# Kernel optimization log

Measured on AMD Instinct MI355X. Metric: run time of the kernel, lower is better.

The kernel has to match this reference:

```python
import jax, jax.numpy as jnp
import numpy as np

DIM = 192
HEADS = 8
TIME = 256
HID = int(DIM * 2.66)  # 510
B, H, W = 4, 128, 128


def conv1x1(x, w, b):
    # w: [O, C], pointwise conv as einsum
    return jnp.einsum('bchw,oc->bohw', x, w) + b[None, :, None, None]


def dwconv3(x, w, b):
    # depthwise 3x3, w: [C, 1, 3, 3]
    y = jax.lax.conv_general_dilated(
        x, w, window_strides=(1, 1), padding='SAME',
        feature_group_count=x.shape[1],
        dimension_numbers=('NCHW', 'OIHW', 'NCHW'))
    return y + b[None, :, None, None]


def layernorm(x, w, b, eps=1e-6):
    # channel-wise LN; torch .std() is unbiased (ddof=1)
    C = x.shape[1]
    mean = x.mean(axis=1, keepdims=True)
    var = ((x - mean) ** 2).sum(axis=1, keepdims=True) / (C - 1)
    std = jnp.sqrt(var)
    return w * (x - mean) / (std + eps) + b


def modulate(x, t_emb, tw, tb):
    # time_mlp = Linear(SiLU(t_emb)); scale/shift conditioning
    t = jax.nn.silu(t_emb) @ tw.T + tb  # [B, 2C]
    scale, shift = jnp.split(t, 2, axis=-1)
    return x * (1.0 + scale[:, :, None, None]) + shift[:, :, None, None]


def l2norm(x, eps=1e-12):
    n = jnp.sqrt((x * x).sum(axis=-1, keepdims=True))
    return x / jnp.maximum(n, eps)


def mdta(x, t_emb, temp, qkv_w, qkv_b, dw_w, dw_b, proj_w, proj_b, tw, tb):
    Bn, C, Hh, Ww = x.shape
    x = modulate(x, t_emb, tw, tb)
    qkv = dwconv3(conv1x1(x, qkv_w, qkv_b), dw_w, dw_b)
    q, k, v = jnp.split(qkv, 3, axis=1)
    rs = lambda a: a.reshape(Bn, HEADS, C // HEADS, Hh * Ww)
    q, k, v = l2norm(rs(q)), l2norm(rs(k)), rs(v)
    attn = jnp.einsum('bhcl,bhdl->bhcd', q, k) * temp[None]  # [B,h,c,c]
    attn = jax.nn.softmax(attn, axis=-1)
    out = jnp.einsum('bhcd,bhdl->bhcl', attn, v).reshape(Bn, C, Hh, Ww)
    return conv1x1(out, proj_w, proj_b)


def gdfn(x, t_emb, c1_w, c1_b, dw_w, dw_b, c2_w, c2_b, tw, tb):
    x = modulate(x, t_emb, tw, tb)
    x = dwconv3(conv1x1(x, c1_w, c1_b), dw_w, dw_b)
    x1, x2 = jnp.split(x, 2, axis=1)
    return conv1x1(x1 * x2, c2_w, c2_b)


def setup_inputs() -> dict:
    key = jax.random.key(0)
    ks = jax.random.split(key, 16)
    s = 0.02
    d = {
        'x': jax.random.normal(ks[0], (B, DIM, H, W), jnp.float32),
        't_emb': jax.random.normal(ks[1], (B, TIME), jnp.float32),
        'n1_w': jnp.ones((1, DIM, 1, 1), jnp.float32),
        'n1_b': jnp.zeros((1, DIM, 1, 1), jnp.float32),
        'temp': jnp.ones((HEADS, 1, 1), jnp.float32),
        'a_qkv_w': jax.random.normal(ks[2], (3 * DIM, DIM), jnp.float32) * s,
        'a_qkv_b': jnp.zeros((3 * DIM,), jnp.float32),
        'a_dw_w': jax.random.normal(ks[3], (3 * DIM, 1, 3, 3), jnp.float32) * s,
        'a_dw_b': jnp.zeros((3 * DIM,), jnp.float32),
        'a_proj_w': jax.random.normal(ks[4], (DIM, DIM), jnp.float32) * s,
        'a_proj_b': jnp.zeros((DIM,), jnp.float32),
        'a_t_w': jax.random.normal(ks[5], (2 * DIM, TIME), jnp.float32) * s,
        'a_t_b': jnp.zeros((2 * DIM,), jnp.float32),
        'n2_w': jnp.ones((1, DIM, 1, 1), jnp.float32),
        'n2_b': jnp.zeros((1, DIM, 1, 1), jnp.float32),
        'f_c1_w': jax.random.normal(ks[6], (2 * HID, DIM), jnp.float32) * s,
        'f_c1_b': jnp.zeros((2 * HID,), jnp.float32),
        'f_dw_w': jax.random.normal(ks[7], (2 * HID, 1, 3, 3), jnp.float32) * s,
        'f_dw_b': jnp.zeros((2 * HID,), jnp.float32),
        'f_c2_w': jax.random.normal(ks[8], (DIM, HID), jnp.float32) * s,
        'f_c2_b': jnp.zeros((DIM,), jnp.float32),
        'f_t_w': jax.random.normal(ks[9], (2 * DIM, TIME), jnp.float32) * s,
        'f_t_b': jnp.zeros((2 * DIM,), jnp.float32),
    }
    return d


def reference(x, t_emb, n1_w, n1_b, temp, a_qkv_w, a_qkv_b, a_dw_w, a_dw_b,
              a_proj_w, a_proj_b, a_t_w, a_t_b, n2_w, n2_b,
              f_c1_w, f_c1_b, f_dw_w, f_dw_b, f_c2_w, f_c2_b, f_t_w, f_t_b):
    x = x + mdta(layernorm(x, n1_w, n1_b), t_emb, temp,
                 a_qkv_w, a_qkv_b, a_dw_w, a_dw_b, a_proj_w, a_proj_b, a_t_w, a_t_b)
    x = x + gdfn(layernorm(x, n2_w, n2_b), t_emb,
                 f_c1_w, f_c1_b, f_dw_w, f_dw_b, f_c2_w, f_c2_b, f_t_w, f_t_b)
    return x
```

## Files before the change

### kernel.cpp

```cpp
#include <hip/hip_runtime.h>
#include <math.h>

#define HW 16384

using short8 = __attribute__((ext_vector_type(8))) short;
using f32x4  = __attribute__((ext_vector_type(4))) float;

__device__ __forceinline__ float bf2f(unsigned short u){
  union { unsigned int i; float f; } x; x.i = ((unsigned int)u) << 16; return x.f;
}
__device__ __forceinline__ unsigned short f2bf(float f){
  union { float f; unsigned int i; } x; x.f = f;
  return (unsigned short)((x.i + 0x7FFFu + ((x.i >> 16) & 1u)) >> 16);
}

__global__ void castw_k(const float* __restrict__ in, unsigned short* __restrict__ out, int n){
  int i = blockIdx.x * 256 + threadIdx.x;
  if (i < n) out[i] = f2bf(in[i]);
}
__global__ void castw_pad_k(const float* __restrict__ in, unsigned short* __restrict__ out,
                            int M, int Kin, int Kout){
  int i = blockIdx.x * 256 + threadIdx.x;
  if (i < M * Kout){
    int m = i / Kout, k = i - m * Kout;
    out[i] = (k < Kin) ? f2bf(in[m * Kin + k]) : (unsigned short)0;
  }
}

__global__ void modk(const float* __restrict__ t_emb,
                     const float* __restrict__ aw, const float* __restrict__ ab,
                     const float* __restrict__ fw, const float* __restrict__ fb,
                     float* __restrict__ mod_a, float* __restrict__ mod_f){
  int o = blockIdx.x * 128 + threadIdx.x;
  int b = blockIdx.y;
  const float* w  = blockIdx.z ? fw : aw;
  const float* bi = blockIdx.z ? fb : ab;
  float* outp     = blockIdx.z ? mod_f : mod_a;
  const float* te = t_emb + b * 256;
  float acc = bi[o];
  for (int k = 0; k < 256; ++k){
    float u = te[k];
    float s = u / (1.f + expf(-u));
    acc += s * w[o * 256 + k];
  }
  outp[b * 384 + o] = acc;
}

__global__ __launch_bounds__(256) void lnmod_k(const float* __restrict__ x,
                                               const float* __restrict__ nw, const float* __restrict__ nb,
                                               const float* __restrict__ mod, unsigned short* __restrict__ y){
  int b = blockIdx.y;
  int p = blockIdx.x * 256 + threadIdx.x;
  const float* xb = x + (size_t)b * 192 * HW + p;
  float s = 0.f, s2 = 0.f;
  #pragma unroll 8
  for (int c = 0; c < 192; ++c){
    float v = xb[(size_t)c * HW]; s += v; s2 += v * v;
  }
  float mean = s * (1.f / 192.f);
  float var  = (s2 - s * mean) * (1.f / 191.f);
  float rinv = 1.f / (sqrtf(fmaxf(var, 0.f)) + 1e-6f);
  const float* mo = mod + b * 384;
  unsigned short* yb = y + ((size_t)b * HW + p) * 192;
  #pragma unroll
  for (int c8 = 0; c8 < 24; ++c8){
    unsigned short ob[8];
    #pragma unroll
    for (int j = 0; j < 8; ++j){
      int c = c8 * 8 + j;
      float v = xb[(size_t)c * HW];
      float ln = nw[c] * ((v - mean) * rinv) + nb[c];
      ob[j] = f2bf(ln * (1.f + mo[c]) + mo[192 + c]);
    }
    *(uint4*)(yb + c8 * 8) = *(const uint4*)ob;
  }
}

__global__ __launch_bounds__(256, 2) void gemm_tn2(const unsigned short* __restrict__ A,
                                                   const unsigned short* __restrict__ Bact,
                                                   const float* __restrict__ bias,
                                                   const float* resid, void* outp,
                                                   int M, int K, int ofp32){
  const int N = HW;
  __shared__ unsigned short SMEM[20480];
  const int m0 = blockIdx.x * 64;
  const int n0 = blockIdx.y * 256;
  const int bz = blockIdx.z;
  const unsigned short* Bp = Bact + (size_t)bz * N * K;
  const int t = threadIdx.x;
  const int w = t >> 6, lane = t & 63;
  const int l16 = lane & 15, quad = lane >> 4;

  const int arow = t >> 2, akc = t & 3;
  int gm = m0 + arow; if (gm > M - 1) gm = M - 1;
  const unsigned short* agp = A + (size_t)gm * K + akc * 8;
  const int aoff = arow * 32 + ((akc ^ ((arow ^ (arow >> 2)) & 3)) * 8);
  const int brow = t >> 2, bkc = t & 3;
  const unsigned short* bgp = Bp + (size_t)(n0 + brow) * K + bkc * 8;
  const int bslot = (bkc ^ ((brow ^ (brow >> 2)) & 3)) * 8;

  f32x4 acc[4][4];
  #pragma unroll
  for (int i = 0; i < 4; ++i)
    #pragma unroll
    for (int j = 0; j < 4; ++j) acc[i][j] = (f32x4){0.f, 0.f, 0.f, 0.f};

  const int kTiles = K >> 5;
  {
    uint4 va = *(const uint4*)agp;
    *(uint4*)&SMEM[aoff] = va;
    #pragma unroll
    for (int i = 0; i < 4; ++i){
      uint4 vb = *(const uint4*)(bgp + (size_t)(64 * i) * K);
      *(uint4*)&SMEM[4096 + (brow + 64 * i) * 32 + bslot] = vb;
    }
  }
  __syncthreads();

  const int fs = (quad ^ ((l16 ^ (l16 >> 2)) & 3)) * 8;
  for (int kt = 0; kt < kTiles; ++kt){
    const int cur = kt & 1;
    const bool more = (kt + 1 < kTiles);
    uint4 va; uint4 vb[4];
    if (more){
      const int k0 = (kt + 1) * 32;
      va = *(const uint4*)(agp + k0);
      #pragma unroll
      for (int i = 0; i < 4; ++i)
        vb[i] = *(const uint4*)(bgp + (size_t)(64 * i) * K + k0);
    }
    const int abase = cur * 2048;
    const int bbase = 4096 + cur * 8192;
    short8 af[4], bfr[4];
    #pragma unroll
    for (int mt = 0; mt < 4; ++mt)
      af[mt] = *(const short8*)&SMEM[abase + (mt * 16 + l16) * 32 + fs];
    #pragma unroll
    for (int nt = 0; nt < 4; ++nt)
      bfr[nt] = *(const short8*)&SMEM[bbase + (w * 64 + nt * 16 + l16) * 32 + fs];
    #pragma unroll
    for (int nt = 0; nt < 4; ++nt)
      #pragma unroll
      for (int mt = 0; mt < 4; ++mt)
        acc[mt][nt] = __builtin_amdgcn_mfma_f32_16x16x32_bf16(af[mt], bfr[nt], acc[mt][nt], 0, 0, 0);
    if (more){
      const int nabase = (cur ^ 1) * 2048;
      const int nbbase = 4096 + (cur ^ 1) * 8192;
      *(uint4*)&SMEM[nabase + aoff] = va;
      #pragma unroll
      for (int i = 0; i < 4; ++i)
        *(uint4*)&SMEM[nbbase + (brow + 64 * i) * 32 + bslot] = vb[i];
    }
    __syncthreads();
  }

  if (!ofp32){
    unsigned short* T = SMEM;
    #pragma unroll
    for (int mt = 0; mt < 4; ++mt)
      #pragma unroll
      for (int nt = 0; nt < 4; ++nt)
        #pragma unroll
        for (int r = 0; r < 4; ++r){
          int ml = mt * 16 + quad * 4 + r;
          int bm = m0 + ml; if (bm > M - 1) bm = M - 1;
          T[ml * 264 + w * 64 + nt * 16 + l16] = f2bf(acc[mt][nt][r] + bias[bm]);
        }
    __syncthreads();
    unsigned short* ob = (unsigned short*)outp + (size_t)bz * M * N;
    #pragma unroll
    for (int i = 0; i < 8; ++i){
      int c = t + 256 * i;
      int row = c >> 5, col = (c & 31) * 8;
      if (m0 + row < M)
        *(uint4*)(ob + (size_t)(m0 + row) * N + n0 + col) = *(const uint4*)&T[row * 264 + col];
    }
  } else {
    float* T = (float*)&SMEM[0];
    float* ob = (float*)outp + (size_t)bz * M * N;
    const float* rb = resid ? resid + (size_t)bz * M * N : nullptr;
    #pragma unroll
    for (int half = 0; half < 2; ++half){
      #pragma unroll
      for (int mt = 0; mt < 2; ++mt)
        #pragma unroll
        for (int nt = 0; nt < 4; ++nt)
          #pragma unroll
          for (int r = 0; r < 4; ++r){
            int ml = mt * 16 + quad * 4 + r;
            T[ml * 260 + w * 64 + nt * 16 + l16] = acc[half * 2 + mt][nt][r];
          }
      __syncthreads();
      #pragma unroll
      for (int i = 0; i < 8; ++i){
        int c = t + 256 * i;
        int row = c >> 6, col = (c & 63) * 4;
        int m = m0 + half * 32 + row;
        if (m < M){
          size_t idx = (size_t)m * N + n0 + col;
          f32x4 v = *(const f32x4*)&T[row * 260 + col];
          float bv = bias[m];
          v[0] += bv; v[1] += bv; v[2] += bv; v[3] += bv;
          if (rb){
            v[0] += rb[idx]; v[1] += rb[idx + 1]; v[2] += rb[idx + 2]; v[3] += rb[idx + 3];
          }
          *(f32x4*)&ob[idx] = v;
        }
      }
      __syncthreads();
    }
  }
}

__global__ __launch_bounds__(256) void dw3_k(const unsigned short* __restrict__ in,
                                             const float* __restrict__ w, const float* __restrict__ bias,
                                             unsigned short* __restrict__ out, int C,
                                             float* __restrict__ qn, float* __restrict__ kn){
  __shared__ unsigned short tile[66 * 128];
  __shared__ float red[4];
  int zc = blockIdx.y;
  int b = zc / C, c = zc - b * C;
  int r0 = blockIdx.x * 64;
  const unsigned short* im = in + ((size_t)(b * C + c)) * HW;
  unsigned short* om = out + ((size_t)(b * C + c)) * HW;
  int t = threadIdx.x;
  #pragma unroll
  for (int i = 0; i < 5; ++i){
    int idx = t + 256 * i;
    if (idx < 1056){
      int lr = idx >> 4, lc = (idx & 15) * 8;
      int gr = r0 - 1 + lr;
      uint4 v = {0u, 0u, 0u, 0u};
      if ((unsigned)gr < 128u) v = *(const uint4*)(im + gr * 128 + lc);
      *(uint4*)&tile[lr * 128 + lc] = v;
    }
  }
  __syncthreads();
  const float* wc = w + c * 9;
  float W[9];
  #pragma unroll
  for (int i = 0; i < 9; ++i) W[i] = wc[i];
  float bs = bias[c];
  float ssq = 0.f;
  #pragma unroll
  for (int i = 0; i < 4; ++i){
    int seg = t + 256 * i;
    int orow = seg >> 4, sc = (seg & 15) * 8;
    float acc[8];
    #pragma unroll
    for (int j = 0; j < 8; ++j) acc[j] = bs;
    #pragma unroll
    for (int rr = 0; rr < 3; ++rr){
      const unsigned short* rp = &tile[(orow + rr) * 128 + sc];
      float v[10];
      v[0] = (sc > 0) ? bf2f(rp[-1]) : 0.f;
      uint4 m = *(const uint4*)rp;
      const unsigned short* mu = (const unsigned short*)&m;
      #pragma unroll
      for (int j = 0; j < 8; ++j) v[j + 1] = bf2f(mu[j]);
      v[9] = (sc < 120) ? bf2f(rp[8]) : 0.f;
      float wa = W[rr * 3], wb = W[rr * 3 + 1], wd = W[rr * 3 + 2];
      #pragma unroll
      for (int j = 0; j < 8; ++j) acc[j] += wa * v[j] + wb * v[j + 1] + wd * v[j + 2];
    }
    unsigned short ob[8];
    #pragma unroll
    for (int j = 0; j < 8; ++j){
      ob[j] = f2bf(acc[j]);
      float q = bf2f(ob[j]);
      ssq += q * q;
    }
    *(uint4*)(om + (r0 + orow) * 128 + sc) = *(uint4*)ob;
  }
  if (c < 384){
    #pragma unroll
    for (int off = 32; off; off >>= 1) ssq += __shfl_down(ssq, off);
    if ((t & 63) == 0) red[t >> 6] = ssq;
    __syncthreads();
    if (t == 0){
      float s = red[0] + red[1] + red[2] + red[3];
      float* dst = (c < 192) ? (qn + b * 192 + c) : (kn + b * 192 + c - 192);
      atomicAdd(dst, s);
    }
  }
}

__global__ __launch_bounds__(256) void dwgate_k(const unsigned short* __restrict__ h,
                                                const float* __restrict__ w, const float* __restrict__ bias,
                                                unsigned short* __restrict__ g){
  __shared__ unsigned short tile[2 * 66 * 128];
  int zc = blockIdx.y;
  int b = zc / 510, j = zc - b * 510;
  int r0 = blockIdx.x * 64;
  const unsigned short* im1 = h + ((size_t)(b * 1020 + j)) * HW;
  const unsigned short* im2 = h + ((size_t)(b * 1020 + 510 + j)) * HW;
  int t = threadIdx.x;
  #pragma unroll
  for (int i = 0; i < 9; ++i){
    int idx = t + 256 * i;
    if (idx < 2112){
      int img = (idx >= 1056) ? 1 : 0;
      int li = idx - img * 1056;
      int lr = li >> 4, lc = (li & 15) * 8;
      int gr = r0 - 1 + lr;
      uint4 v = {0u, 0u, 0u, 0u};
      const unsigned short* im = img ? im2 : im1;
      if ((unsigned)gr < 128u) v = *(const uint4*)(im + gr * 128 + lc);
      *(uint4*)&tile[img * 8448 + lr * 128 + lc] = v;
    }
  }
  __syncthreads();
  float W1[9], W2[9];
  #pragma unroll
  for (int i = 0; i < 9; ++i){ W1[i] = w[j * 9 + i]; W2[i] = w[(510 + j) * 9 + i]; }
  float b1 = bias[j], b2 = bias[510 + j];
  unsigned short* gm = g + ((size_t)(b * 510 + j)) * HW;
  #pragma unroll
  for (int i = 0; i < 4; ++i){
    int seg = t + 256 * i;
    int orow = seg >> 4, sc = (seg & 15) * 8;
    float a1[8], a2[8];
    #pragma unroll
    for (int q = 0; q < 8; ++q){ a1[q] = b1; a2[q] = b2; }
    #pragma unroll
    for (int rr = 0; rr < 3; ++rr){
      #pragma unroll
      for (int img = 0; img < 2; ++img){
        const unsigned short* rp = &tile[img * 8448 + (orow + rr) * 128 + sc];
        float v[10];
        v[0] = (sc > 0) ? bf2f(rp[-1]) : 0.f;
        uint4 m = *(const uint4*)rp;
        const unsigned short* mu = (const unsigned short*)&m;
        #pragma unroll
        for (int q = 0; q < 8; ++q) v[q + 1] = bf2f(mu[q]);
        v[9] = (sc < 120) ? bf2f(rp[8]) : 0.f;
        const float* ww = img ? W2 : W1;
        float* aa = img ? a2 : a1;
        float wa = ww[rr * 3], wb = ww[rr * 3 + 1], wd = ww[rr * 3 + 2];
        #pragma unroll
        for (int q = 0; q < 8; ++q) aa[q] += wa * v[q] + wb * v[q + 1] + wd * v[q + 2];
      }
    }
    unsigned short ob[8];
    #pragma unroll
    for (int q = 0; q < 8; ++q) ob[q] = f2bf(a1[q] * a2[q]);
    *(uint4*)(gm + (r0 + orow) * 128 + sc) = *(uint4*)ob;
  }
}

__global__ __launch_bounds__(256) void tr_k(const unsigned short* __restrict__ in,
                                            unsigned short* __restrict__ out, int C, int Kout){
  __shared__ unsigned short tile[64 * 72];
  int b = blockIdx.z;
  int p0 = blockIdx.x * 64, c0 = blockIdx.y * 64;
  int t = threadIdx.x;
  #pragma unroll
  for (int i = 0; i < 2; ++i){
    int id = t + 256 * i;
    int ch = id >> 3, pc = (id & 7) * 8;
    uint4 v = {0u, 0u, 0u, 0u};
    if (c0 + ch < C) v = *(const uint4*)(in + ((size_t)(b * C + c0 + ch)) * HW + p0 + pc);
    const unsigned short* u = (const unsigned short*)&v;
    #pragma unroll
    for (int j = 0; j < 8; ++j) tile[(pc + j) * 72 + ch] = u[j];
  }
  __syncthreads();
  #pragma unroll
  for (int i = 0; i < 2; ++i){
    int id = t + 256 * i;
    int px = id >> 3, cc = (id & 7) * 8;
    *(uint4*)(out + ((size_t)b * HW + p0 + px) * Kout + c0 + cc) = *(const uint4*)&tile[px * 72 + cc];
  }
}

__global__ __launch_bounds__(64) void qk_k(const unsigned short* __restrict__ qkv_dw, float* __restrict__ part){
  int bh = blockIdx.y; int b = bh >> 3, h = bh & 7;
  int ks = blockIdx.x;
  int lane = threadIdx.x;
  int l16 = lane & 15, quad = lane >> 4;
  const unsigned short* qb = qkv_dw + ((size_t)b * 576 + h * 24) * HW;
  const unsigned short* kb = qkv_dw + ((size_t)b * 576 + 192 + h * 24) * HW;
  f32x4 z = {0.f, 0.f, 0.f, 0.f};
  f32x4 a00 = z, a01 = z, a10 = z, a11 = z;
  for (int st = 0; st < 16; ++st){
    int k0 = ks * 512 + st * 32 + quad * 8;
    short8 qa0 = *(const short8*)(qb + (size_t)l16 * HW + k0);
    short8 qa1 = *(const short8*)(qb + (size_t)(l16 + 16) * HW + k0);
    short8 kb0 = *(const short8*)(kb + (size_t)l16 * HW + k0);
    short8 kb1 = *(const short8*)(kb + (size_t)(l16 + 16) * HW + k0);
    a00 = __builtin_amdgcn_mfma_f32_16x16x32_bf16(qa0, kb0, a00, 0, 0, 0);
    a01 = __builtin_amdgcn_mfma_f32_16x16x32_bf16(qa0, kb1, a01, 0, 0, 0);
    a10 = __builtin_amdgcn_mfma_f32_16x16x32_bf16(qa1, kb0, a10, 0, 0, 0);
    a11 = __builtin_amdgcn_mfma_f32_16x16x32_bf16(qa1, kb1, a11, 0, 0, 0);
  }
  float* pp = part + ((size_t)bh * 32 + ks) * 576;
  #pragma unroll
  for (int r = 0; r < 4; ++r){
    int c0 = quad * 4 + r, c1 = 16 + quad * 4 + r;
    int d0 = l16, d1 = 16 + l16;
    if (c0 < 24 && d0 < 24) pp[c0 * 24 + d0] = a00[r];
    if (c0 < 24 && d1 < 24) pp[c0 * 24 + d1] = a01[r];
    if (c1 < 24 && d0 < 24) pp[c1 * 24 + d0] = a10[r];
    if (c1 < 24 && d1 < 24) pp[c1 * 24 + d1] = a11[r];
  }
}

__global__ void softmax_k(const float* __restrict__ part, const float* __restrict__ qn,
                          const float* __restrict__ kn, const float* __restrict__ temp,
                          float* __restrict__ attn){
  int bh = blockIdx.x; int b = bh >> 3, h = bh & 7;
  int c = threadIdx.x;
  if (c >= 24) return;
  float tmp = temp[h];
  float qv = fmaxf(sqrtf(qn[b * 192 + h * 24 + c]), 1e-12f);
  float row[24];
  #pragma unroll
  for (int d = 0; d < 24; ++d){
    float s = 0.f;
    for (int sp = 0; sp < 32; ++sp) s += part[((size_t)bh * 32 + sp) * 576 + c * 24 + d];
    float kv = fmaxf(sqrtf(kn[b * 192 + h * 24 + d]), 1e-12f);
    row[d] = s * tmp / (qv * kv);
  }
  float mx = row[0];
  #pragma unroll
  for (int d = 1; d < 24; ++d) mx = fmaxf(mx, row[d]);
  float sum = 0.f;
  #pragma unroll
  for (int d = 0; d < 24; ++d){ row[d] = expf(row[d] - mx); sum += row[d]; }
  float inv = 1.f / sum;
  #pragma unroll
  for (int d = 0; d < 24; ++d) attn[(size_t)bh * 576 + c * 24 + d] = row[d] * inv;
}

__global__ __launch_bounds__(256) void av_k(const float* __restrict__ attn,
                                            const unsigned short* __restrict__ qkv_dw,
                                            unsigned short* __restrict__ o){
  int bh = blockIdx.y; int b = bh >> 3, h = bh & 7;
  __shared__ float As[576];
  int t = threadIdx.x;
  for (int i = t; i < 576; i += 256) As[i] = attn[(size_t)bh * 576 + i];
  __syncthreads();
  int p = blockIdx.x * 256 + t;
  const unsigned short* vb = qkv_dw + ((size_t)b * 576 + 384 + h * 24) * HW + p;
  float acc[24];
  #pragma unroll
  for (int c = 0; c < 24; ++c) acc[c] = 0.f;
  #pragma unroll
  for (int d = 0; d < 24; ++d){
    float vv = bf2f(vb[(size_t)d * HW]);
    #pragma unroll
    for (int c = 0; c < 24; ++c) acc[c] += As[c * 24 + d] * vv;
  }
  unsigned short ob[24];
  #pragma unroll
  for (int c = 0; c < 24; ++c) ob[c] = f2bf(acc[c]);
  unsigned short* op = o + ((size_t)b * HW + p) * 192 + h * 24;
  #pragma unroll
  for (int i = 0; i < 3; ++i) *(uint4*)(op + i * 8) = *(const uint4*)(ob + i * 8);
}

extern "C" void kernel_launch(void* const* d_in, const int* in_sizes, int n_in,
                              void* d_out, int out_size, void* d_ws, size_t ws_size,
                              hipStream_t stream){
  (void)in_sizes; (void)n_in; (void)out_size; (void)ws_size;
  const float* x        = (const float*)d_in[0];
  const float* t_emb    = (const float*)d_in[1];
  const float* n1_w     = (const float*)d_in[2];
  const float* n1_b     = (const float*)d_in[3];
  const float* temp     = (const float*)d_in[4];
  const float* a_qkv_w  = (const float*)d_in[5];
  const float* a_qkv_b  = (const float*)d_in[6];
  const float* a_dw_w   = (const float*)d_in[7];
  const float* a_dw_b   = (const float*)d_in[8];
  const float* a_proj_w = (const float*)d_in[9];
  const float* a_proj_b = (const float*)d_in[10];
  const float* a_t_w    = (const float*)d_in[11];
  const float* a_t_b    = (const float*)d_in[12];
  const float* n2_w     = (const float*)d_in[13];
  const float* n2_b     = (const float*)d_in[14];
  const float* f_c1_w   = (const float*)d_in[15];
  const float* f_c1_b   = (const float*)d_in[16];
  const float* f_dw_w   = (const float*)d_in[17];
  const float* f_dw_b   = (const float*)d_in[18];
  const float* f_c2_w   = (const float*)d_in[19];
  const float* f_c2_b   = (const float*)d_in[20];
  const float* f_t_w    = (const float*)d_in[21];
  const float* f_t_b    = (const float*)d_in[22];
  float* out = (float*)d_out;
  char* ws = (char*)d_ws;

  unsigned short* y_buf = (unsigned short*)(ws + 0);
  unsigned short* qkv   = (unsigned short*)(ws + 25165824);
  unsigned short* hbuf  = (unsigned short*)(ws + 25165824);
  unsigned short* gbufT = (unsigned short*)(ws + 25165824);
  unsigned short* qkvd  = (unsigned short*)(ws + 100663296);
  unsigned short* obuf  = (unsigned short*)(ws + 176160768);
  unsigned short* gbuf  = (unsigned short*)(ws + 158859264);
  const size_t S = 225705984;
  float* mod_a = (float*)(ws + S);
  float* mod_f = (float*)(ws + S + 8192);
  float* qn    = (float*)(ws + S + 16384);
  float* kn    = (float*)(ws + S + 20480);
  float* part  = (float*)(ws + S + 24576);
  float* attn  = (float*)(ws + S + 2383872);
  unsigned short* Wq  = (unsigned short*)(ws + S + 2457600);
  unsigned short* Wp  = (unsigned short*)(ws + S + 2678784);
  unsigned short* W1  = (unsigned short*)(ws + S + 2752512);
  unsigned short* W2p = (unsigned short*)(ws + S + 3144192);

  castw_k<<<dim3((110592 + 255) / 256), 256, 0, stream>>>(a_qkv_w, Wq, 110592);
  castw_k<<<dim3((36864 + 255) / 256), 256, 0, stream>>>(a_proj_w, Wp, 36864);
  castw_k<<<dim3((195840 + 255) / 256), 256, 0, stream>>>(f_c1_w, W1, 195840);
  castw_pad_k<<<dim3((98304 + 255) / 256), 256, 0, stream>>>(f_c2_w, W2p, 192, 510, 512);
  modk<<<dim3(3, 4, 2), 128, 0, stream>>>(t_emb, a_t_w, a_t_b, f_t_w, f_t_b, mod_a, mod_f);
  (void)hipMemsetAsync(qn, 0, 2 * 768 * sizeof(float), stream);

  lnmod_k<<<dim3(64, 4), 256, 0, stream>>>(x, n1_w, n1_b, mod_a, y_buf);
  gemm_tn2<<<dim3(9, 64, 4), 256, 0, stream>>>(Wq, y_buf, a_qkv_b, nullptr, qkv, 576, 192, 0);
  dw3_k<<<dim3(2, 2304), 256, 0, stream>>>(qkv, a_dw_w, a_dw_b, qkvd, 576, qn, kn);
  qk_k<<<dim3(32, 32), 64, 0, stream>>>(qkvd, part);
  softmax_k<<<32, 64, 0, stream>>>(part, qn, kn, temp, attn);
  av_k<<<dim3(64, 32), 256, 0, stream>>>(attn, qkvd, obuf);
  gemm_tn2<<<dim3(3, 64, 4), 256, 0, stream>>>(Wp, obuf, a_proj_b, x, out, 192, 192, 1);

  lnmod_k<<<dim3(64, 4), 256, 0, stream>>>(out, n2_w, n2_b, mod_f, y_buf);
  gemm_tn2<<<dim3(16, 64, 4), 256, 0, stream>>>(W1, y_buf, f_c1_b, nullptr, hbuf, 1020, 192, 0);
  dwgate_k<<<dim3(2, 2040), 256, 0, stream>>>(hbuf, f_dw_w, f_dw_b, gbuf);
  tr_k<<<dim3(256, 8, 4), 256, 0, stream>>>(gbuf, gbufT, 510, 512);
  gemm_tn2<<<dim3(3, 64, 4), 256, 0, stream>>>(W2p, gbufT, f_c2_b, out, out, 192, 512, 1);
}
```

Baseline: 780.4 us.

## Retile pointwise GEMM to 256 output channels by 64 pixels per block

Changes the bf16 MFMA GEMM block tile from 64 output channels by 256 pixels to 256 channels by 64 pixels. Each wave now owns 64 channel rows instead of 64 pixel columns, and the shared-memory staging and both epilogues are reworked to match. Launch grids shrink along the channel axis and grow along the pixel axis. The large activation matrix is therefore re-read fewer times, at the cost of wasted MFMA work on padded channel rows when M is 192 or 576, and shorter 128-byte row segments in the output stores.

```diff
diff --git a/kernel.cpp b/kernel.cpp
--- a/kernel.cpp
+++ b/kernel.cpp
@@ -83,8 +83,8 @@
                                                    int M, int K, int ofp32){
   const int N = HW;
   __shared__ unsigned short SMEM[20480];
-  const int m0 = blockIdx.x * 64;
-  const int n0 = blockIdx.y * 256;
+  const int m0 = blockIdx.x * 256;
+  const int n0 = blockIdx.y * 64;
   const int bz = blockIdx.z;
   const unsigned short* Bp = Bact + (size_t)bz * N * K;
   const int t = threadIdx.x;
@@ -92,12 +92,16 @@
   const int l16 = lane & 15, quad = lane >> 4;
 
   const int arow = t >> 2, akc = t & 3;
-  int gm = m0 + arow; if (gm > M - 1) gm = M - 1;
-  const unsigned short* agp = A + (size_t)gm * K + akc * 8;
+  const unsigned short* agp[4];
+  #pragma unroll
+  for (int i = 0; i < 4; ++i){
+    int gm = m0 + arow + 64 * i; if (gm > M - 1) gm = M - 1;
+    agp[i] = A + (size_t)gm * K + akc * 8;
+  }
   const int aoff = arow * 32 + ((akc ^ ((arow ^ (arow >> 2)) & 3)) * 8);
   const int brow = t >> 2, bkc = t & 3;
   const unsigned short* bgp = Bp + (size_t)(n0 + brow) * K + bkc * 8;
-  const int bslot = (bkc ^ ((brow ^ (brow >> 2)) & 3)) * 8;
+  const int boff = brow * 32 + ((bkc ^ ((brow ^ (brow >> 2)) & 3)) * 8);
 
   f32x4 acc[4][4];
   #pragma unroll
@@ -107,13 +111,10 @@
 
   const int kTiles = K >> 5;
   {
-    uint4 va = *(const uint4*)agp;
-    *(uint4*)&SMEM[aoff] = va;
-    #pragma unroll
-    for (int i = 0; i < 4; ++i){
-      uint4 vb = *(const uint4*)(bgp + (size_t)(64 * i) * K);
-      *(uint4*)&SMEM[4096 + (brow + 64 * i) * 32 + bslot] = vb;
-    }
+    #pragma unroll
+    for (int i = 0; i < 4; ++i)
+      *(uint4*)&SMEM[i * 2048 + aoff] = *(const uint4*)agp[i];
+    *(uint4*)&SMEM[16384 + boff] = *(const uint4*)bgp;
   }
   __syncthreads();
 
@@ -121,35 +122,34 @@
   for (int kt = 0; kt < kTiles; ++kt){
     const int cur = kt & 1;
     const bool more = (kt + 1 < kTiles);
-    uint4 va; uint4 vb[4];
+    uint4 va[4]; uint4 vb;
     if (more){
       const int k0 = (kt + 1) * 32;
-      va = *(const uint4*)(agp + k0);
-      #pragma unroll
-      for (int i = 0; i < 4; ++i)
-        vb[i] = *(const uint4*)(bgp + (size_t)(64 * i) * K + k0);
-    }
-    const int abase = cur * 2048;
-    const int bbase = 4096 + cur * 8192;
+      #pragma unroll
+      for (int i = 0; i < 4; ++i) va[i] = *(const uint4*)(agp[i] + k0);
+      vb = *(const uint4*)(bgp + k0);
+    }
+    const int abase = cur * 8192;
+    const int bbase = 16384 + cur * 2048;
     short8 af[4], bfr[4];
     #pragma unroll
     for (int mt = 0; mt < 4; ++mt)
-      af[mt] = *(const short8*)&SMEM[abase + (mt * 16 + l16) * 32 + fs];
+      af[mt] = *(const short8*)&SMEM[abase + (w * 64 + mt * 16 + l16) * 32 + fs];
     #pragma unroll
     for (int nt = 0; nt < 4; ++nt)
-      bfr[nt] = *(const short8*)&SMEM[bbase + (w * 64 + nt * 16 + l16) * 32 + fs];
+      bfr[nt] = *(const short8*)&SMEM[bbase + (nt * 16 + l16) * 32 + fs];
     #pragma unroll
     for (int nt = 0; nt < 4; ++nt)
       #pragma unroll
       for (int mt = 0; mt < 4; ++mt)
         acc[mt][nt] = __builtin_amdgcn_mfma_f32_16x16x32_bf16(af[mt], bfr[nt], acc[mt][nt], 0, 0, 0);
     if (more){
-      const int nabase = (cur ^ 1) * 2048;
-      const int nbbase = 4096 + (cur ^ 1) * 8192;
-      *(uint4*)&SMEM[nabase + aoff] = va;
+      const int nabase = (cur ^ 1) * 8192;
+      const int nbbase = 16384 + (cur ^ 1) * 2048;
       #pragma unroll
       for (int i = 0; i < 4; ++i)
-        *(uint4*)&SMEM[nbbase + (brow + 64 * i) * 32 + bslot] = vb[i];
+        *(uint4*)&SMEM[nabase + i * 2048 + aoff] = va[i];
+      *(uint4*)&SMEM[nbbase + boff] = vb;
     }
     __syncthreads();
   }
@@ -162,18 +162,18 @@
       for (int nt = 0; nt < 4; ++nt)
         #pragma unroll
         for (int r = 0; r < 4; ++r){
-          int ml = mt * 16 + quad * 4 + r;
+          int ml = w * 64 + mt * 16 + quad * 4 + r;
           int bm = m0 + ml; if (bm > M - 1) bm = M - 1;
-          T[ml * 264 + w * 64 + nt * 16 + l16] = f2bf(acc[mt][nt][r] + bias[bm]);
+          T[ml * 72 + nt * 16 + l16] = f2bf(acc[mt][nt][r] + bias[bm]);
         }
     __syncthreads();
     unsigned short* ob = (unsigned short*)outp + (size_t)bz * M * N;
     #pragma unroll
     for (int i = 0; i < 8; ++i){
       int c = t + 256 * i;
-      int row = c >> 5, col = (c & 31) * 8;
+      int row = c >> 3, col = (c & 7) * 8;
       if (m0 + row < M)
-        *(uint4*)(ob + (size_t)(m0 + row) * N + n0 + col) = *(const uint4*)&T[row * 264 + col];
+        *(uint4*)(ob + (size_t)(m0 + row) * N + n0 + col) = *(const uint4*)&T[row * 72 + col];
     }
   } else {
     float* T = (float*)&SMEM[0];
@@ -181,24 +181,26 @@
     const float* rb = resid ? resid + (size_t)bz * M * N : nullptr;
     #pragma unroll
     for (int half = 0; half < 2; ++half){
-      #pragma unroll
-      for (int mt = 0; mt < 2; ++mt)
+      if ((w >> 1) == half){
         #pragma unroll
-        for (int nt = 0; nt < 4; ++nt)
+        for (int mt = 0; mt < 4; ++mt)
           #pragma unroll
-          for (int r = 0; r < 4; ++r){
-            int ml = mt * 16 + quad * 4 + r;
-            T[ml * 260 + w * 64 + nt * 16 + l16] = acc[half * 2 + mt][nt][r];
-          }
+          for (int nt = 0; nt < 4; ++nt)
+            #pragma unroll
+            for (int r = 0; r < 4; ++r){
+              int ml = (w & 1) * 64 + mt * 16 + quad * 4 + r;
+              T[ml * 68 + nt * 16 + l16] = acc[mt][nt][r];
+            }
+      }
       __syncthreads();
       #pragma unroll
       for (int i = 0; i < 8; ++i){
         int c = t + 256 * i;
-        int row = c >> 6, col = (c & 63) * 4;
-        int m = m0 + half * 32 + row;
+        int row = c >> 4, col = (c & 15) * 4;
+        int m = m0 + half * 128 + row;
         if (m < M){
           size_t idx = (size_t)m * N + n0 + col;
-          f32x4 v = *(const f32x4*)&T[row * 260 + col];
+          f32x4 v = *(const f32x4*)&T[row * 68 + col];
           float bv = bias[m];
           v[0] += bv; v[1] += bv; v[2] += bv; v[3] += bv;
           if (rb){
@@ -516,16 +518,16 @@
   (void)hipMemsetAsync(qn, 0, 2 * 768 * sizeof(float), stream);
 
   lnmod_k<<<dim3(64, 4), 256, 0, stream>>>(x, n1_w, n1_b, mod_a, y_buf);
-  gemm_tn2<<<dim3(9, 64, 4), 256, 0, stream>>>(Wq, y_buf, a_qkv_b, nullptr, qkv, 576, 192, 0);
+  gemm_tn2<<<dim3(3, 256, 4), 256, 0, stream>>>(Wq, y_buf, a_qkv_b, nullptr, qkv, 576, 192, 0);
   dw3_k<<<dim3(2, 2304), 256, 0, stream>>>(qkv, a_dw_w, a_dw_b, qkvd, 576, qn, kn);
   qk_k<<<dim3(32, 32), 64, 0, stream>>>(qkvd, part);
   softmax_k<<<32, 64, 0, stream>>>(part, qn, kn, temp, attn);
   av_k<<<dim3(64, 32), 256, 0, stream>>>(attn, qkvd, obuf);
-  gemm_tn2<<<dim3(3, 64, 4), 256, 0, stream>>>(Wp, obuf, a_proj_b, x, out, 192, 192, 1);
+  gemm_tn2<<<dim3(1, 256, 4), 256, 0, stream>>>(Wp, obuf, a_proj_b, x, out, 192, 192, 1);
 
   lnmod_k<<<dim3(64, 4), 256, 0, stream>>>(out, n2_w, n2_b, mod_f, y_buf);
-  gemm_tn2<<<dim3(16, 64, 4), 256, 0, stream>>>(W1, y_buf, f_c1_b, nullptr, hbuf, 1020, 192, 0);
+  gemm_tn2<<<dim3(4, 256, 4), 256, 0, stream>>>(W1, y_buf, f_c1_b, nullptr, hbuf, 1020, 192, 0);
   dwgate_k<<<dim3(2, 2040), 256, 0, stream>>>(hbuf, f_dw_w, f_dw_b, gbuf);
   tr_k<<<dim3(256, 8, 4), 256, 0, stream>>>(gbuf, gbufT, 510, 512);
-  gemm_tn2<<<dim3(3, 64, 4), 256, 0, stream>>>(W2p, gbufT, f_c2_b, out, out, 192, 512, 1);
-}
+  gemm_tn2<<<dim3(1, 256, 4), 256, 0, stream>>>(W2p, gbufT, f_c2_b, out, out, 192, 512, 1);
+}
```

After: 770.9 us. No clear change (-1.2%).
